# Kernel optimization log

Measured on AMD Instinct MI355X. Metric: run time of the kernel, lower is better.

The kernel has to match this reference:

```python
import jax, jax.numpy as jnp
import numpy as np

RADIUS = 0.1
NSAMPLE = 32


def ball_query_cnt(radius, nsample, xyz, new_xyz):
    """xyz: (B,N,3), new_xyz: (B,npoint,3) -> cnt (B,npoint) int32, idx (B,npoint,nsample) int32.
    Matches pointnet2 CUDA semantics: first `nsample` in-radius points in index order;
    unfilled slots replicate the first found index (0 if none found)."""
    N = xyz.shape[1]
    # (B, npoint, N) squared distances
    d2 = jnp.sum((new_xyz[:, :, None, :] - xyz[:, None, :, :]) ** 2, axis=-1)
    mask = d2 < radius * radius
    pos = jnp.arange(N, dtype=jnp.int32)
    # key encodes position so that top_k returns the LOWEST valid positions first
    key = jnp.where(mask, N - pos, -N)
    topk_vals, _ = jax.lax.top_k(key, nsample)          # (B, npoint, nsample)
    valid = topk_vals > 0
    idx = (N - topk_vals).astype(jnp.int32)
    first = jnp.where(valid[..., :1], idx[..., :1], 0)   # fill value per query
    idx = jnp.where(valid, idx, first)
    cnt = jnp.minimum(mask.sum(axis=-1), nsample).astype(jnp.int32)
    return cnt, idx


def group(features, idx):
    """features: (B,C,N), idx: (B,npoint,nsample) -> (B,C,npoint,nsample)."""
    return jax.vmap(lambda f, i: f[:, i])(features, idx)


def setup_inputs() -> dict:
    key = jax.random.key(0)
    k1, k2, k3 = jax.random.split(key, 3)
    B, N, npoint, C = 4, 16384, 2048, 64
    xyz = jax.random.uniform(k1, (B, N, 3), dtype=jnp.float32)
    new_xyz = jax.random.uniform(k2, (B, npoint, 3), dtype=jnp.float32)
    features = jax.random.normal(k3, (B, C, N), dtype=jnp.float32)
    return {"xyz": xyz, "new_xyz": new_xyz, "features": features}


def reference(xyz, new_xyz, features):
    idx_cnt, idx = ball_query_cnt(RADIUS, NSAMPLE, xyz, new_xyz)
    xyz_t = jnp.transpose(xyz, (0, 2, 1))                      # (B,3,N)
    grouped_xyz = group(xyz_t, idx)                            # (B,3,npoint,nsample)
    grouped_xyz = grouped_xyz - jnp.transpose(new_xyz, (0, 2, 1))[..., None]
    grouped_features = group(features, idx)                    # (B,C,npoint,nsample)
    new_features = jnp.concatenate([grouped_xyz, grouped_features], axis=1)
    return idx_cnt, new_features
```

## Files before the change

kernel.cpp:

```cpp
#include <hip/hip_runtime.h>

#define B        4
#define N        16384
#define NPOINT   2048
#define C        64
#define NSAMPLE  32
#define CH       (C + 3)
#define RADIUS2  0.01f
#define NCELL    1000
#define CSTRIDE  1032
#define CCSTRIDE 1024
#define CAP      256

__device__ __forceinline__ int clamp10(int v) {
    return v < 0 ? 0 : (v > 9 ? 9 : v);
}

__global__ __launch_bounds__(256) void zero_kernel(int* __restrict__ p, int n) {
    const int i = blockIdx.x * 256 + threadIdx.x;
    if (i < n) p[i] = 0;
}

__global__ __launch_bounds__(256) void count_kernel(const float* __restrict__ xyz,
                                                    int* __restrict__ cnt) {
    const int g = blockIdx.x * 256 + threadIdx.x;
    const int b = g >> 14;
    const float x = xyz[g * 3 + 0], y = xyz[g * 3 + 1], z = xyz[g * 3 + 2];
    const int cx = clamp10((int)(x * 10.f));
    const int cy = clamp10((int)(y * 10.f));
    const int cz = clamp10((int)(z * 10.f));
    atomicAdd(&cnt[(b << 10) + (cx * 10 + cy) * 10 + cz], 1);
}

__global__ __launch_bounds__(1024) void prefix_kernel(int* __restrict__ cnt,
                                                      int* __restrict__ cs) {
    __shared__ int s[1024];
    const int t = threadIdx.x, b = blockIdx.x;
    const int v = (t < NCELL) ? cnt[(b << 10) + t] : 0;
    s[t] = v;
    __syncthreads();
    for (int off = 1; off < 1024; off <<= 1) {
        const int u = (t >= off) ? s[t - off] : 0;
        __syncthreads();
        s[t] += u;
        __syncthreads();
    }
    const int excl = (t == 0) ? 0 : s[t - 1];
    if (t <= NCELL) cs[b * CSTRIDE + t] = excl;
    if (t < NCELL)  cnt[(b << 10) + t] = excl;
}

__global__ __launch_bounds__(256) void scatter_kernel(const float* __restrict__ xyz,
                                                      int* __restrict__ cursor,
                                                      float4* __restrict__ sp) {
    const int g = blockIdx.x * 256 + threadIdx.x;
    const int b = g >> 14;
    const int n = g & (N - 1);
    const float x = xyz[g * 3 + 0], y = xyz[g * 3 + 1], z = xyz[g * 3 + 2];
    const int cx = clamp10((int)(x * 10.f));
    const int cy = clamp10((int)(y * 10.f));
    const int cz = clamp10((int)(z * 10.f));
    const int cell = (cx * 10 + cy) * 10 + cz;
    const int pos = atomicAdd(&cursor[(b << 10) + cell], 1);
    sp[(b << 14) + pos] = make_float4(x, y, z, __int_as_float(n));
}

__global__ __launch_bounds__(256) void feat_transpose_kernel(
    const float* __restrict__ f,
    float* __restrict__ ft)
{
    __shared__ float tile[64][65];
    const int b  = blockIdx.y;
    const int n0 = blockIdx.x * 64;
    const int t  = threadIdx.x;
    const int r16 = t >> 4;
    const int x4  = t & 15;
    #pragma unroll
    for (int it = 0; it < 4; ++it) {
        const int cc = it * 16 + r16;
        const float4 v = *(const float4*)(f + ((size_t)b * C + cc) * N + n0 + x4 * 4);
        tile[cc][x4 * 4 + 0] = v.x;
        tile[cc][x4 * 4 + 1] = v.y;
        tile[cc][x4 * 4 + 2] = v.z;
        tile[cc][x4 * 4 + 3] = v.w;
    }
    __syncthreads();
    #pragma unroll
    for (int it = 0; it < 4; ++it) {
        const int nn = it * 16 + r16;
        float4 v;
        v.x = tile[x4 * 4 + 0][nn];
        v.y = tile[x4 * 4 + 1][nn];
        v.z = tile[x4 * 4 + 2][nn];
        v.w = tile[x4 * 4 + 3][nn];
        *(float4*)(ft + ((size_t)b * N + n0 + nn) * C + x4 * 4) = v;
    }
}

__global__ __launch_bounds__(64) void qg_grid_kernel(
    const float*  __restrict__ xyz,
    const float*  __restrict__ new_xyz,
    const float*  __restrict__ ft,
    const int*    __restrict__ cs,
    const float4* __restrict__ sp,
    float* __restrict__ out_cnt,
    float* __restrict__ out_feat)
{
    const int q = blockIdx.x;
    const int b = q >> 11;
    const int j = q & (NPOINT - 1);
    const int l = threadIdx.x;

    __shared__ int   cand[CAP];
    __shared__ int   s_idx[NSAMPLE];
    __shared__ float s_tile[CH * 33];

    const float qx = new_xyz[q * 3 + 0];
    const float qy = new_xyz[q * 3 + 1];
    const float qz = new_xyz[q * 3 + 2];

    const int cx = clamp10((int)(qx * 10.f));
    const int cy = clamp10((int)(qy * 10.f));
    const int cz = clamp10((int)(qz * 10.f));
    const int z0 = cz > 0 ? cz - 1 : 0;
    const int z1 = cz < 9 ? cz + 1 : 9;

    int sv = 0, ev = 0;
    if (l < 9) {
        const int xx = cx - 1 + l / 3;
        const int yy = cy - 1 + l % 3;
        if (xx >= 0 && xx <= 9 && yy >= 0 && yy <= 9) {
            const int cb = (xx * 10 + yy) * 10;
            sv = cs[b * CSTRIDE + cb + z0];
            ev = cs[b * CSTRIDE + cb + z1 + 1];
        }
    }

    const unsigned long long ltmask = (1ull << l) - 1ull;
    int total = 0, ncand = 0;
    for (int r = 0; r < 9; ++r) {
        const int rs = __shfl(sv, r);
        const int re = __shfl(ev, r);
        for (int p0 = rs; p0 < re; p0 += 64) {
            const int p = p0 + l;
            const bool act = p < re;
            float4 pt = make_float4(1e9f, 1e9f, 1e9f, 0.f);
            if (act) pt = sp[(b << 14) + p];
            const float dx = pt.x - qx, dy = pt.y - qy, dz = pt.z - qz;
            const float d2 = dx * dx + dy * dy + dz * dz;
            const bool in = act && (d2 < RADIUS2);
            const unsigned long long m = __ballot(in);
            if (in) {
                const int slot = ncand + __popcll(m & ltmask);
                if (slot < CAP) cand[slot] = __float_as_int(pt.w);
            }
            const int c = __popcll(m);
            total += c;
            ncand = ncand + c > CAP ? CAP : ncand + c;
        }
    }

    int cntv;
    if (total > CAP) {
        const float* xb = xyz + (size_t)b * N * 3;
        int cnt2 = 0;
        for (int base = 0; base < N; base += 64) {
            const int p = base + l;
            const float dx = xb[p * 3 + 0] - qx;
            const float dy = xb[p * 3 + 1] - qy;
            const float dz = xb[p * 3 + 2] - qz;
            const float d2 = dx * dx + dy * dy + dz * dz;
            const bool in = d2 < RADIUS2;
            const unsigned long long m = __ballot(in);
            if (in) {
                const int slot = cnt2 + __popcll(m & ltmask);
                if (slot < NSAMPLE) s_idx[slot] = p;
            }
            cnt2 += __popcll(m);
            if (cnt2 >= NSAMPLE) break;
        }
        cntv = cnt2 < NSAMPLE ? cnt2 : NSAMPLE;
        __syncthreads();
    } else {
        __syncthreads();
        const int K = ncand;
        for (int c = l; c < K; c += 64) {
            const int v = cand[c];
            int rnk = 0;
            for (int i = 0; i < K; ++i) rnk += (cand[i] < v) ? 1 : 0;
            if (rnk < NSAMPLE) s_idx[rnk] = v;
        }
        cntv = total < NSAMPLE ? total : NSAMPLE;
        __syncthreads();
    }

    if (l == 0) out_cnt[q] = (float)cntv;
    if (l < NSAMPLE && l >= cntv) s_idx[l] = (cntv > 0) ? s_idx[0] : 0;
    __syncthreads();

    #pragma unroll
    for (int p = 0; p < 8; ++p) {
        const int k  = p * 4 + (l >> 4);
        const int c4 = l & 15;
        const int i  = s_idx[k];
        const float4 v = ((const float4*)(ft + ((size_t)b * N + i) * C))[c4];
        const int ch = 3 + c4 * 4;
        s_tile[(ch + 0) * 33 + k] = v.x;
        s_tile[(ch + 1) * 33 + k] = v.y;
        s_tile[(ch + 2) * 33 + k] = v.z;
        s_tile[(ch + 3) * 33 + k] = v.w;
    }
    if (l < NSAMPLE) {
        const int i = s_idx[l];
        const float* xp = xyz + ((size_t)b * N + i) * 3;
        s_tile[0 * 33 + l] = xp[0] - qx;
        s_tile[1 * 33 + l] = xp[1] - qy;
        s_tile[2 * 33 + l] = xp[2] - qz;
    }
    __syncthreads();

    float4* of4 = (float4*)out_feat;
    for (int e4 = l; e4 < CH * 8; e4 += 64) {
        const int ch = e4 >> 3;
        const int k4 = e4 & 7;
        float4 v;
        v.x = s_tile[ch * 33 + k4 * 4 + 0];
        v.y = s_tile[ch * 33 + k4 * 4 + 1];
        v.z = s_tile[ch * 33 + k4 * 4 + 2];
        v.w = s_tile[ch * 33 + k4 * 4 + 3];
        of4[((size_t)(b * CH + ch) * NPOINT + j) * 8 + k4] = v;
    }
}

template <bool TRANSPOSED>
__global__ __launch_bounds__(64) void qg_wave_kernel(
    const float* __restrict__ xyz,
    const float* __restrict__ new_xyz,
    const float* __restrict__ feat,
    float* __restrict__ out_cnt,
    float* __restrict__ out_feat)
{
    const int q = blockIdx.x;
    const int b = q >> 11;
    const int j = q & (NPOINT - 1);
    const int l = threadIdx.x;

    __shared__ int   s_idx[NSAMPLE];
    __shared__ float s_tile[CH * 33];

    const float qx = new_xyz[q * 3 + 0];
    const float qy = new_xyz[q * 3 + 1];
    const float qz = new_xyz[q * 3 + 2];
    const float* xb = xyz + (size_t)b * N * 3;

    int cnt = 0;
    for (int base = 0; base < N; base += 64) {
        const int p = base + l;
        const float dx = xb[p * 3 + 0] - qx;
        const float dy = xb[p * 3 + 1] - qy;
        const float dz = xb[p * 3 + 2] - qz;
        const float d2 = dx * dx + dy * dy + dz * dz;
        const bool in = d2 < RADIUS2;
        const unsigned long long m = __ballot(in);
        if (in) {
            const int slot = cnt + __popcll(m & ((1ull << l) - 1ull));
            if (slot < NSAMPLE) s_idx[slot] = p;
        }
        cnt += __popcll(m);
        if (cnt >= NSAMPLE) break;
    }
    if (cnt > NSAMPLE) cnt = NSAMPLE;

    if (l == 0) out_cnt[q] = (float)cnt;
    __syncthreads();
    if (l < NSAMPLE && l >= cnt) s_idx[l] = (cnt > 0) ? s_idx[0] : 0;
    __syncthreads();

    #pragma unroll
    for (int p = 0; p < 8; ++p) {
        const int k  = p * 4 + (l >> 4);
        const int c4 = l & 15;
        const int i  = s_idx[k];
        if (TRANSPOSED) {
            const float4 v = ((const float4*)(feat + ((size_t)b * N + i) * C))[c4];
            const int ch = 3 + c4 * 4;
            s_tile[(ch + 0) * 33 + k] = v.x;
            s_tile[(ch + 1) * 33 + k] = v.y;
            s_tile[(ch + 2) * 33 + k] = v.z;
            s_tile[(ch + 3) * 33 + k] = v.w;
        } else {
            #pragma unroll
            for (int cc = 0; cc < 4; ++cc) {
                const int c = c4 * 4 + cc;
                s_tile[(3 + c) * 33 + k] = feat[((size_t)b * C + c) * N + i];
            }
        }
    }
    if (l < NSAMPLE) {
        const int i = s_idx[l];
        const float* xp = xyz + ((size_t)b * N + i) * 3;
        s_tile[0 * 33 + l] = xp[0] - qx;
        s_tile[1 * 33 + l] = xp[1] - qy;
        s_tile[2 * 33 + l] = xp[2] - qz;
    }
    __syncthreads();

    float4* of4 = (float4*)out_feat;
    for (int e4 = l; e4 < CH * 8; e4 += 64) {
        const int ch = e4 >> 3;
        const int k4 = e4 & 7;
        float4 v;
        v.x = s_tile[ch * 33 + k4 * 4 + 0];
        v.y = s_tile[ch * 33 + k4 * 4 + 1];
        v.z = s_tile[ch * 33 + k4 * 4 + 2];
        v.w = s_tile[ch * 33 + k4 * 4 + 3];
        of4[((size_t)(b * CH + ch) * NPOINT + j) * 8 + k4] = v;
    }
}

extern "C" void kernel_launch(void* const* d_in, const int* in_sizes, int n_in,
                              void* d_out, int out_size, void* d_ws, size_t ws_size,
                              hipStream_t stream) {
    const float* xyz      = (const float*)d_in[0];
    const float* new_xyz  = (const float*)d_in[1];
    const float* features = (const float*)d_in[2];

    float* out_cnt  = (float*)d_out;
    float* out_feat = out_cnt + (size_t)B * NPOINT;

    char* ws = (char*)d_ws;
    const size_t ftB = (size_t)B * N * C * sizeof(float);
    const size_t spB = (size_t)B * N * sizeof(float4);
    const size_t csB = (size_t)B * CSTRIDE * sizeof(int);
    const size_t ccB = (size_t)B * CCSTRIDE * sizeof(int);
    const size_t need = ftB + spB + csB + ccB;

    if (ws_size >= need) {
        float*  ft = (float*)ws;
        float4* sp = (float4*)(ws + ftB);
        int*    cs = (int*)(ws + ftB + spB);
        int*    cc = (int*)(ws + ftB + spB + csB);
        zero_kernel<<<(B * CCSTRIDE + 255) / 256, 256, 0, stream>>>(cc, B * CCSTRIDE);
        count_kernel<<<B * N / 256, 256, 0, stream>>>(xyz, cc);
        prefix_kernel<<<B, 1024, 0, stream>>>(cc, cs);
        scatter_kernel<<<B * N / 256, 256, 0, stream>>>(xyz, cc, sp);
        feat_transpose_kernel<<<dim3(N / 64, B), 256, 0, stream>>>(features, ft);
        qg_grid_kernel<<<B * NPOINT, 64, 0, stream>>>(xyz, new_xyz, ft, cs, sp,
                                                      out_cnt, out_feat);
    } else if (ws_size >= ftB) {
        float* ft = (float*)ws;
        feat_transpose_kernel<<<dim3(N / 64, B), 256, 0, stream>>>(features, ft);
        qg_wave_kernel<true><<<B * NPOINT, 64, 0, stream>>>(xyz, new_xyz, ft,
                                                            out_cnt, out_feat);
    } else {
        qg_wave_kernel<false><<<B * NPOINT, 64, 0, stream>>>(xyz, new_xyz, features,
                                                             out_cnt, out_feat);
    }
}
```

Before: 126.3 us.

## Split ball query from grouping, flatten cell scan, pack four queries per block

The fused query+group kernel becomes two kernels: a ball-query kernel that writes indices to a workspace buffer, and a group kernel that gathers features. Both run four wave-sized queries per 256-thread block with per-wave shared memory, replacing __syncthreads with block fences. The 9-cell candidate scan is flattened into one loop over the concatenated ranges to cut partial-wave iterations. Zeroing of the cell counters is folded into the feature transpose kernel, the candidate cap is reduced, and outputs use nontemporal stores. The extra index round trip through global memory and the reliance on wave-level ordering in place of barriers are the costs and risks.

```diff
diff --git a/kernel.cpp b/kernel.cpp
--- a/kernel.cpp
+++ b/kernel.cpp
@@ -10,15 +10,48 @@
 #define NCELL    1000
 #define CSTRIDE  1032
 #define CCSTRIDE 1024
-#define CAP      256
+#define CAP      192
+
+typedef float vfloat4 __attribute__((ext_vector_type(4)));
 
 __device__ __forceinline__ int clamp10(int v) {
     return v < 0 ? 0 : (v > 9 ? 9 : v);
 }
 
-__global__ __launch_bounds__(256) void zero_kernel(int* __restrict__ p, int n) {
-    const int i = blockIdx.x * 256 + threadIdx.x;
-    if (i < n) p[i] = 0;
+__global__ __launch_bounds__(256) void feat_transpose_zero_kernel(
+    const float* __restrict__ f,
+    float* __restrict__ ft,
+    int* __restrict__ cc)
+{
+    if (blockIdx.y == 0 && blockIdx.x < (B * CCSTRIDE) / 256)
+        cc[blockIdx.x * 256 + threadIdx.x] = 0;
+
+    __shared__ float tile[64][65];
+    const int b  = blockIdx.y;
+    const int n0 = blockIdx.x * 64;
+    const int t  = threadIdx.x;
+    const int r16 = t >> 4;
+    const int x4  = t & 15;
+    #pragma unroll
+    for (int it = 0; it < 4; ++it) {
+        const int cc_ = it * 16 + r16;
+        const float4 v = *(const float4*)(f + ((size_t)b * C + cc_) * N + n0 + x4 * 4);
+        tile[cc_][x4 * 4 + 0] = v.x;
+        tile[cc_][x4 * 4 + 1] = v.y;
+        tile[cc_][x4 * 4 + 2] = v.z;
+        tile[cc_][x4 * 4 + 3] = v.w;
+    }
+    __syncthreads();
+    #pragma unroll
+    for (int it = 0; it < 4; ++it) {
+        const int nn = it * 16 + r16;
+        float4 v;
+        v.x = tile[x4 * 4 + 0][nn];
+        v.y = tile[x4 * 4 + 1][nn];
+        v.z = tile[x4 * 4 + 2][nn];
+        v.w = tile[x4 * 4 + 3][nn];
+        *(float4*)(ft + ((size_t)b * N + n0 + nn) * C + x4 * 4) = v;
+    }
 }
 
 __global__ __launch_bounds__(256) void count_kernel(const float* __restrict__ xyz,
@@ -65,55 +98,23 @@
     sp[(b << 14) + pos] = make_float4(x, y, z, __int_as_float(n));
 }
 
-__global__ __launch_bounds__(256) void feat_transpose_kernel(
-    const float* __restrict__ f,
-    float* __restrict__ ft)
-{
-    __shared__ float tile[64][65];
-    const int b  = blockIdx.y;
-    const int n0 = blockIdx.x * 64;
-    const int t  = threadIdx.x;
-    const int r16 = t >> 4;
-    const int x4  = t & 15;
-    #pragma unroll
-    for (int it = 0; it < 4; ++it) {
-        const int cc = it * 16 + r16;
-        const float4 v = *(const float4*)(f + ((size_t)b * C + cc) * N + n0 + x4 * 4);
-        tile[cc][x4 * 4 + 0] = v.x;
-        tile[cc][x4 * 4 + 1] = v.y;
-        tile[cc][x4 * 4 + 2] = v.z;
-        tile[cc][x4 * 4 + 3] = v.w;
-    }
-    __syncthreads();
-    #pragma unroll
-    for (int it = 0; it < 4; ++it) {
-        const int nn = it * 16 + r16;
-        float4 v;
-        v.x = tile[x4 * 4 + 0][nn];
-        v.y = tile[x4 * 4 + 1][nn];
-        v.z = tile[x4 * 4 + 2][nn];
-        v.w = tile[x4 * 4 + 3][nn];
-        *(float4*)(ft + ((size_t)b * N + n0 + nn) * C + x4 * 4) = v;
-    }
-}
-
-__global__ __launch_bounds__(64) void qg_grid_kernel(
+__global__ __launch_bounds__(256, 8) void ballquery_kernel(
     const float*  __restrict__ xyz,
     const float*  __restrict__ new_xyz,
-    const float*  __restrict__ ft,
     const int*    __restrict__ cs,
     const float4* __restrict__ sp,
     float* __restrict__ out_cnt,
-    float* __restrict__ out_feat)
+    int*   __restrict__ idx_out)
 {
-    const int q = blockIdx.x;
+    const int w = threadIdx.x >> 6;
+    const int l = threadIdx.x & 63;
+    const int q = blockIdx.x * 4 + w;
     const int b = q >> 11;
-    const int j = q & (NPOINT - 1);
-    const int l = threadIdx.x;
-
-    __shared__ int   cand[CAP];
-    __shared__ int   s_idx[NSAMPLE];
-    __shared__ float s_tile[CH * 33];
+
+    __shared__ int cand_s[4][CAP];
+    __shared__ int sidx_s[4][NSAMPLE];
+    int* cand  = cand_s[w];
+    int* s_idx = sidx_s[w];
 
     const float qx = new_xyz[q * 3 + 0];
     const float qy = new_xyz[q * 3 + 1];
@@ -135,29 +136,43 @@
             ev = cs[b * CSTRIDE + cb + z1 + 1];
         }
     }
+    const int len = ev - sv;
+
+    int S[9], L[9];
+    #pragma unroll
+    for (int r = 0; r < 9; ++r) {
+        S[r] = __builtin_amdgcn_readlane(sv, r);
+        L[r] = __builtin_amdgcn_readlane(len, r);
+    }
+    int T = 0;
+    #pragma unroll
+    for (int r = 0; r < 9; ++r) T += L[r];
 
     const unsigned long long ltmask = (1ull << l) - 1ull;
     int total = 0, ncand = 0;
-    for (int r = 0; r < 9; ++r) {
-        const int rs = __shfl(sv, r);
-        const int re = __shfl(ev, r);
-        for (int p0 = rs; p0 < re; p0 += 64) {
-            const int p = p0 + l;
-            const bool act = p < re;
-            float4 pt = make_float4(1e9f, 1e9f, 1e9f, 0.f);
-            if (act) pt = sp[(b << 14) + p];
-            const float dx = pt.x - qx, dy = pt.y - qy, dz = pt.z - qz;
-            const float d2 = dx * dx + dy * dy + dz * dz;
-            const bool in = act && (d2 < RADIUS2);
-            const unsigned long long m = __ballot(in);
-            if (in) {
-                const int slot = ncand + __popcll(m & ltmask);
-                if (slot < CAP) cand[slot] = __float_as_int(pt.w);
-            }
-            const int c = __popcll(m);
-            total += c;
-            ncand = ncand + c > CAP ? CAP : ncand + c;
-        }
+    for (int base = 0; base < T; base += 64) {
+        const int wid = base + l;
+        int p = 0, acc = 0;
+        bool act = false;
+        #pragma unroll
+        for (int r = 0; r < 9; ++r) {
+            const int off = wid - acc;
+            if (off >= 0 && off < L[r]) { p = S[r] + off; act = true; }
+            acc += L[r];
+        }
+        float4 pt = make_float4(1e9f, 1e9f, 1e9f, 0.f);
+        if (act) pt = sp[(b << 14) + p];
+        const float dx = pt.x - qx, dy = pt.y - qy, dz = pt.z - qz;
+        const float d2 = dx * dx + dy * dy + dz * dz;
+        const bool in = act && (d2 < RADIUS2);
+        const unsigned long long m = __ballot(in);
+        if (in) {
+            const int slot = ncand + __popcll(m & ltmask);
+            if (slot < CAP) cand[slot] = __float_as_int(pt.w);
+        }
+        const int c = __popcll(m);
+        total += c;
+        ncand = ncand + c > CAP ? CAP : ncand + c;
     }
 
     int cntv;
@@ -180,9 +195,9 @@
             if (cnt2 >= NSAMPLE) break;
         }
         cntv = cnt2 < NSAMPLE ? cnt2 : NSAMPLE;
-        __syncthreads();
+        __threadfence_block();
     } else {
-        __syncthreads();
+        __threadfence_block();
         const int K = ncand;
         for (int c = l; c < K; c += 64) {
             const int v = cand[c];
@@ -191,12 +206,36 @@
             if (rnk < NSAMPLE) s_idx[rnk] = v;
         }
         cntv = total < NSAMPLE ? total : NSAMPLE;
-        __syncthreads();
-    }
+        __threadfence_block();
+    }
+
+    if (l < NSAMPLE && l >= cntv) s_idx[l] = (cntv > 0) ? s_idx[0] : 0;
+    __threadfence_block();
 
     if (l == 0) out_cnt[q] = (float)cntv;
-    if (l < NSAMPLE && l >= cntv) s_idx[l] = (cntv > 0) ? s_idx[0] : 0;
-    __syncthreads();
+    if (l < NSAMPLE) idx_out[q * NSAMPLE + l] = s_idx[l];
+}
+
+__global__ __launch_bounds__(256, 4) void group_kernel(
+    const float* __restrict__ xyz,
+    const float* __restrict__ new_xyz,
+    const float* __restrict__ ft,
+    const int*   __restrict__ idx_in,
+    float* __restrict__ out_feat)
+{
+    const int w = threadIdx.x >> 6;
+    const int l = threadIdx.x & 63;
+    const int q = blockIdx.x * 4 + w;
+    const int b = q >> 11;
+    const int j = q & (NPOINT - 1);
+
+    __shared__ float tile_s[4][CH * 33];
+    __shared__ int   sidx_s[4][NSAMPLE];
+    float* s_tile = tile_s[w];
+    int*   s_idx  = sidx_s[w];
+
+    if (l < NSAMPLE) s_idx[l] = idx_in[q * NSAMPLE + l];
+    __threadfence_block();
 
     #pragma unroll
     for (int p = 0; p < 8; ++p) {
@@ -211,24 +250,27 @@
         s_tile[(ch + 3) * 33 + k] = v.w;
     }
     if (l < NSAMPLE) {
+        const float qx = new_xyz[q * 3 + 0];
+        const float qy = new_xyz[q * 3 + 1];
+        const float qz = new_xyz[q * 3 + 2];
         const int i = s_idx[l];
         const float* xp = xyz + ((size_t)b * N + i) * 3;
         s_tile[0 * 33 + l] = xp[0] - qx;
         s_tile[1 * 33 + l] = xp[1] - qy;
         s_tile[2 * 33 + l] = xp[2] - qz;
     }
-    __syncthreads();
-
-    float4* of4 = (float4*)out_feat;
+    __threadfence_block();
+
+    vfloat4* of4 = (vfloat4*)out_feat;
     for (int e4 = l; e4 < CH * 8; e4 += 64) {
         const int ch = e4 >> 3;
         const int k4 = e4 & 7;
-        float4 v;
+        vfloat4 v;
         v.x = s_tile[ch * 33 + k4 * 4 + 0];
         v.y = s_tile[ch * 33 + k4 * 4 + 1];
         v.z = s_tile[ch * 33 + k4 * 4 + 2];
         v.w = s_tile[ch * 33 + k4 * 4 + 3];
-        of4[((size_t)(b * CH + ch) * NPOINT + j) * 8 + k4] = v;
+        __builtin_nontemporal_store(v, &of4[((size_t)(b * CH + ch) * NPOINT + j) * 8 + k4]);
     }
 }
 
@@ -329,27 +371,31 @@
     float* out_feat = out_cnt + (size_t)B * NPOINT;
 
     char* ws = (char*)d_ws;
-    const size_t ftB = (size_t)B * N * C * sizeof(float);
-    const size_t spB = (size_t)B * N * sizeof(float4);
-    const size_t csB = (size_t)B * CSTRIDE * sizeof(int);
-    const size_t ccB = (size_t)B * CCSTRIDE * sizeof(int);
-    const size_t need = ftB + spB + csB + ccB;
+    const size_t ftB  = (size_t)B * N * C * sizeof(float);
+    const size_t spB  = (size_t)B * N * sizeof(float4);
+    const size_t csB  = (size_t)B * CSTRIDE * sizeof(int);
+    const size_t ccB  = (size_t)B * CCSTRIDE * sizeof(int);
+    const size_t idxB = (size_t)B * NPOINT * NSAMPLE * sizeof(int);
+    const size_t need = ftB + spB + csB + ccB + idxB;
 
     if (ws_size >= need) {
-        float*  ft = (float*)ws;
-        float4* sp = (float4*)(ws + ftB);
-        int*    cs = (int*)(ws + ftB + spB);
-        int*    cc = (int*)(ws + ftB + spB + csB);
-        zero_kernel<<<(B * CCSTRIDE + 255) / 256, 256, 0, stream>>>(cc, B * CCSTRIDE);
+        float*  ft  = (float*)ws;
+        float4* sp  = (float4*)(ws + ftB);
+        int*    cs  = (int*)(ws + ftB + spB);
+        int*    cc  = (int*)(ws + ftB + spB + csB);
+        int*    idx = (int*)(ws + ftB + spB + csB + ccB);
+        feat_transpose_zero_kernel<<<dim3(N / 64, B), 256, 0, stream>>>(features, ft, cc);
         count_kernel<<<B * N / 256, 256, 0, stream>>>(xyz, cc);
         prefix_kernel<<<B, 1024, 0, stream>>>(cc, cs);
         scatter_kernel<<<B * N / 256, 256, 0, stream>>>(xyz, cc, sp);
-        feat_transpose_kernel<<<dim3(N / 64, B), 256, 0, stream>>>(features, ft);
-        qg_grid_kernel<<<B * NPOINT, 64, 0, stream>>>(xyz, new_xyz, ft, cs, sp,
-                                                      out_cnt, out_feat);
+        ballquery_kernel<<<B * NPOINT / 4, 256, 0, stream>>>(xyz, new_xyz, cs, sp,
+                                                             out_cnt, idx);
+        group_kernel<<<B * NPOINT / 4, 256, 0, stream>>>(xyz, new_xyz, ft, idx,
+                                                         out_feat);
     } else if (ws_size >= ftB) {
         float* ft = (float*)ws;
-        feat_transpose_kernel<<<dim3(N / 64, B), 256, 0, stream>>>(features, ft);
+        feat_transpose_zero_kernel<<<dim3(N / 64, B), 256, 0, stream>>>(
+            features, ft, (int*)(ws + ftB - (size_t)B * CCSTRIDE * sizeof(int)));
         qg_wave_kernel<true><<<B * NPOINT, 64, 0, stream>>>(xyz, new_xyz, ft,
                                                             out_cnt, out_feat);
     } else {
```

Result: slower. 133.5 us (+5.7%).

## Fuse grid-build and transpose into one prep kernel, pack four queries per block

Applied to the files above, without the earlier changes.

The zero, count, prefix, scatter and feature-transpose kernels are merged into one prep kernel. Four blocks build each batch's cell histogram, prefix sum and scatter in shared memory, and the remaining blocks do the transpose. The query kernel now runs four one-wave queries per 256-thread block, with wave-local fences in place of block barriers. It walks the nine cell ranges as one flattened loop, uses a smaller candidate cap, and writes output with nontemporal stores. The goal is to cut launch overhead and global atomics and to improve occupancy. In exchange, the per-batch serial histogram block runs with little parallelism, and correctness now relies on single-wave LDS ordering.

```diff
diff --git a/kernel.cpp b/kernel.cpp
--- a/kernel.cpp
+++ b/kernel.cpp
@@ -9,95 +9,105 @@
 #define RADIUS2  0.01f
 #define NCELL    1000
 #define CSTRIDE  1032
-#define CCSTRIDE 1024
-#define CAP      256
+#define CAP      192
+
+typedef float vfloat4 __attribute__((ext_vector_type(4)));
 
 __device__ __forceinline__ int clamp10(int v) {
     return v < 0 ? 0 : (v > 9 ? 9 : v);
 }
 
-__global__ __launch_bounds__(256) void zero_kernel(int* __restrict__ p, int n) {
-    const int i = blockIdx.x * 256 + threadIdx.x;
-    if (i < n) p[i] = 0;
-}
-
-__global__ __launch_bounds__(256) void count_kernel(const float* __restrict__ xyz,
-                                                    int* __restrict__ cnt) {
-    const int g = blockIdx.x * 256 + threadIdx.x;
-    const int b = g >> 14;
-    const float x = xyz[g * 3 + 0], y = xyz[g * 3 + 1], z = xyz[g * 3 + 2];
-    const int cx = clamp10((int)(x * 10.f));
-    const int cy = clamp10((int)(y * 10.f));
-    const int cz = clamp10((int)(z * 10.f));
-    atomicAdd(&cnt[(b << 10) + (cx * 10 + cy) * 10 + cz], 1);
-}
-
-__global__ __launch_bounds__(1024) void prefix_kernel(int* __restrict__ cnt,
-                                                      int* __restrict__ cs) {
-    __shared__ int s[1024];
-    const int t = threadIdx.x, b = blockIdx.x;
-    const int v = (t < NCELL) ? cnt[(b << 10) + t] : 0;
-    s[t] = v;
-    __syncthreads();
-    for (int off = 1; off < 1024; off <<= 1) {
-        const int u = (t >= off) ? s[t - off] : 0;
-        __syncthreads();
-        s[t] += u;
-        __syncthreads();
-    }
-    const int excl = (t == 0) ? 0 : s[t - 1];
-    if (t <= NCELL) cs[b * CSTRIDE + t] = excl;
-    if (t < NCELL)  cnt[(b << 10) + t] = excl;
-}
-
-__global__ __launch_bounds__(256) void scatter_kernel(const float* __restrict__ xyz,
-                                                      int* __restrict__ cursor,
-                                                      float4* __restrict__ sp) {
-    const int g = blockIdx.x * 256 + threadIdx.x;
-    const int b = g >> 14;
-    const int n = g & (N - 1);
-    const float x = xyz[g * 3 + 0], y = xyz[g * 3 + 1], z = xyz[g * 3 + 2];
-    const int cx = clamp10((int)(x * 10.f));
-    const int cy = clamp10((int)(y * 10.f));
-    const int cz = clamp10((int)(z * 10.f));
-    const int cell = (cx * 10 + cy) * 10 + cz;
-    const int pos = atomicAdd(&cursor[(b << 10) + cell], 1);
-    sp[(b << 14) + pos] = make_float4(x, y, z, __int_as_float(n));
-}
-
-__global__ __launch_bounds__(256) void feat_transpose_kernel(
+__global__ __launch_bounds__(256) void prep_kernel(
+    const float* __restrict__ xyz,
     const float* __restrict__ f,
-    float* __restrict__ ft)
+    float* __restrict__ ft,
+    int* __restrict__ cs,
+    float4* __restrict__ sp)
 {
-    __shared__ float tile[64][65];
-    const int b  = blockIdx.y;
-    const int n0 = blockIdx.x * 64;
-    const int t  = threadIdx.x;
-    const int r16 = t >> 4;
-    const int x4  = t & 15;
-    #pragma unroll
-    for (int it = 0; it < 4; ++it) {
-        const int cc = it * 16 + r16;
-        const float4 v = *(const float4*)(f + ((size_t)b * C + cc) * N + n0 + x4 * 4);
-        tile[cc][x4 * 4 + 0] = v.x;
-        tile[cc][x4 * 4 + 1] = v.y;
-        tile[cc][x4 * 4 + 2] = v.z;
-        tile[cc][x4 * 4 + 3] = v.w;
-    }
-    __syncthreads();
-    #pragma unroll
-    for (int it = 0; it < 4; ++it) {
-        const int nn = it * 16 + r16;
-        float4 v;
-        v.x = tile[x4 * 4 + 0][nn];
-        v.y = tile[x4 * 4 + 1][nn];
-        v.z = tile[x4 * 4 + 2][nn];
-        v.w = tile[x4 * 4 + 3][nn];
-        *(float4*)(ft + ((size_t)b * N + n0 + nn) * C + x4 * 4) = v;
-    }
-}
-
-__global__ __launch_bounds__(64) void qg_grid_kernel(
+    const int t = threadIdx.x;
+
+    if (blockIdx.x < B) {
+        const int b = blockIdx.x;
+        const float* xb = xyz + (size_t)b * N * 3;
+
+        __shared__ int hist[1024];
+        __shared__ int wsum[256];
+
+        hist[t] = 0; hist[256 + t] = 0; hist[512 + t] = 0; hist[768 + t] = 0;
+        __syncthreads();
+
+        for (int g = t; g < N; g += 256) {
+            const int cx = clamp10((int)(xb[g * 3 + 0] * 10.f));
+            const int cy = clamp10((int)(xb[g * 3 + 1] * 10.f));
+            const int cz = clamp10((int)(xb[g * 3 + 2] * 10.f));
+            atomicAdd(&hist[(cx * 10 + cy) * 10 + cz], 1);
+        }
+        __syncthreads();
+
+        const int h0 = hist[t * 4 + 0], h1 = hist[t * 4 + 1];
+        const int h2 = hist[t * 4 + 2], h3 = hist[t * 4 + 3];
+        wsum[t] = h0 + h1 + h2 + h3;
+        __syncthreads();
+        for (int off = 1; off < 256; off <<= 1) {
+            const int u = (t >= off) ? wsum[t - off] : 0;
+            __syncthreads();
+            wsum[t] += u;
+            __syncthreads();
+        }
+        const int base = (t == 0) ? 0 : wsum[t - 1];
+        const int c0 = base, c1 = c0 + h0, c2 = c1 + h1, c3 = c2 + h2;
+        __syncthreads();
+        hist[t * 4 + 0] = c0;
+        hist[t * 4 + 1] = c1;
+        hist[t * 4 + 2] = c2;
+        hist[t * 4 + 3] = c3;
+        int* csb = cs + b * CSTRIDE;
+        csb[t * 4 + 0] = c0;
+        csb[t * 4 + 1] = c1;
+        csb[t * 4 + 2] = c2;
+        csb[t * 4 + 3] = c3;
+        __syncthreads();
+
+        for (int g = t; g < N; g += 256) {
+            const float x = xb[g * 3 + 0], y = xb[g * 3 + 1], z = xb[g * 3 + 2];
+            const int cx = clamp10((int)(x * 10.f));
+            const int cy = clamp10((int)(y * 10.f));
+            const int cz = clamp10((int)(z * 10.f));
+            const int pos = atomicAdd(&hist[(cx * 10 + cy) * 10 + cz], 1);
+            sp[(b << 14) + pos] = make_float4(x, y, z, __int_as_float(g));
+        }
+    } else {
+        const int tt = blockIdx.x - B;
+        const int b  = tt >> 8;
+        const int n0 = (tt & 255) * 64;
+
+        __shared__ float tile[64][65];
+        const int r16 = t >> 4;
+        const int x4  = t & 15;
+        #pragma unroll
+        for (int it = 0; it < 4; ++it) {
+            const int cc = it * 16 + r16;
+            const float4 v = *(const float4*)(f + ((size_t)b * C + cc) * N + n0 + x4 * 4);
+            tile[cc][x4 * 4 + 0] = v.x;
+            tile[cc][x4 * 4 + 1] = v.y;
+            tile[cc][x4 * 4 + 2] = v.z;
+            tile[cc][x4 * 4 + 3] = v.w;
+        }
+        __syncthreads();
+        #pragma unroll
+        for (int it = 0; it < 4; ++it) {
+            const int nn = it * 16 + r16;
+            float4 v;
+            v.x = tile[x4 * 4 + 0][nn];
+            v.y = tile[x4 * 4 + 1][nn];
+            v.z = tile[x4 * 4 + 2][nn];
+            v.w = tile[x4 * 4 + 3][nn];
+            *(float4*)(ft + ((size_t)b * N + n0 + nn) * C + x4 * 4) = v;
+        }
+    }
+}
+
+__global__ __launch_bounds__(256, 4) void qg_kernel(
     const float*  __restrict__ xyz,
     const float*  __restrict__ new_xyz,
     const float*  __restrict__ ft,
@@ -106,14 +116,18 @@
     float* __restrict__ out_cnt,
     float* __restrict__ out_feat)
 {
-    const int q = blockIdx.x;
+    const int w = threadIdx.x >> 6;
+    const int l = threadIdx.x & 63;
+    const int q = blockIdx.x * 4 + w;
     const int b = q >> 11;
     const int j = q & (NPOINT - 1);
-    const int l = threadIdx.x;
-
-    __shared__ int   cand[CAP];
-    __shared__ int   s_idx[NSAMPLE];
-    __shared__ float s_tile[CH * 33];
+
+    __shared__ int   cand_s[4][CAP];
+    __shared__ int   sidx_s[4][NSAMPLE];
+    __shared__ float tile_s[4][CH * 33];
+    int*   cand   = cand_s[w];
+    int*   s_idx  = sidx_s[w];
+    float* s_tile = tile_s[w];
 
     const float qx = new_xyz[q * 3 + 0];
     const float qy = new_xyz[q * 3 + 1];
@@ -135,29 +149,43 @@
             ev = cs[b * CSTRIDE + cb + z1 + 1];
         }
     }
+    const int len = ev - sv;
+
+    int S[9], L[9];
+    #pragma unroll
+    for (int r = 0; r < 9; ++r) {
+        S[r] = __builtin_amdgcn_readlane(sv, r);
+        L[r] = __builtin_amdgcn_readlane(len, r);
+    }
+    int T = 0;
+    #pragma unroll
+    for (int r = 0; r < 9; ++r) T += L[r];
 
     const unsigned long long ltmask = (1ull << l) - 1ull;
     int total = 0, ncand = 0;
-    for (int r = 0; r < 9; ++r) {
-        const int rs = __shfl(sv, r);
-        const int re = __shfl(ev, r);
-        for (int p0 = rs; p0 < re; p0 += 64) {
-            const int p = p0 + l;
-            const bool act = p < re;
-            float4 pt = make_float4(1e9f, 1e9f, 1e9f, 0.f);
-            if (act) pt = sp[(b << 14) + p];
-            const float dx = pt.x - qx, dy = pt.y - qy, dz = pt.z - qz;
-            const float d2 = dx * dx + dy * dy + dz * dz;
-            const bool in = act && (d2 < RADIUS2);
-            const unsigned long long m = __ballot(in);
-            if (in) {
-                const int slot = ncand + __popcll(m & ltmask);
-                if (slot < CAP) cand[slot] = __float_as_int(pt.w);
-            }
-            const int c = __popcll(m);
-            total += c;
-            ncand = ncand + c > CAP ? CAP : ncand + c;
-        }
+    for (int base = 0; base < T; base += 64) {
+        const int wid = base + l;
+        int p = 0, acc = 0;
+        bool act = false;
+        #pragma unroll
+        for (int r = 0; r < 9; ++r) {
+            const int off = wid - acc;
+            if (off >= 0 && off < L[r]) { p = S[r] + off; act = true; }
+            acc += L[r];
+        }
+        float4 pt = make_float4(1e9f, 1e9f, 1e9f, 0.f);
+        if (act) pt = sp[(b << 14) + p];
+        const float dx = pt.x - qx, dy = pt.y - qy, dz = pt.z - qz;
+        const float d2 = dx * dx + dy * dy + dz * dz;
+        const bool in = act && (d2 < RADIUS2);
+        const unsigned long long m = __ballot(in);
+        if (in) {
+            const int slot = ncand + __popcll(m & ltmask);
+            if (slot < CAP) cand[slot] = __float_as_int(pt.w);
+        }
+        const int c = __popcll(m);
+        total += c;
+        ncand = ncand + c > CAP ? CAP : ncand + c;
     }
 
     int cntv;
@@ -180,9 +208,9 @@
             if (cnt2 >= NSAMPLE) break;
         }
         cntv = cnt2 < NSAMPLE ? cnt2 : NSAMPLE;
-        __syncthreads();
+        __threadfence_block();
     } else {
-        __syncthreads();
+        __threadfence_block();
         const int K = ncand;
         for (int c = l; c < K; c += 64) {
             const int v = cand[c];
@@ -191,12 +219,13 @@
             if (rnk < NSAMPLE) s_idx[rnk] = v;
         }
         cntv = total < NSAMPLE ? total : NSAMPLE;
-        __syncthreads();
-    }
+        __threadfence_block();
+    }
+
+    if (l < NSAMPLE && l >= cntv) s_idx[l] = (cntv > 0) ? s_idx[0] : 0;
+    __threadfence_block();
 
     if (l == 0) out_cnt[q] = (float)cntv;
-    if (l < NSAMPLE && l >= cntv) s_idx[l] = (cntv > 0) ? s_idx[0] : 0;
-    __syncthreads();
 
     #pragma unroll
     for (int p = 0; p < 8; ++p) {
@@ -217,22 +246,21 @@
         s_tile[1 * 33 + l] = xp[1] - qy;
         s_tile[2 * 33 + l] = xp[2] - qz;
     }
-    __syncthreads();
-
-    float4* of4 = (float4*)out_feat;
+    __threadfence_block();
+
+    vfloat4* of4 = (vfloat4*)out_feat;
     for (int e4 = l; e4 < CH * 8; e4 += 64) {
         const int ch = e4 >> 3;
         const int k4 = e4 & 7;
-        float4 v;
+        vfloat4 v;
         v.x = s_tile[ch * 33 + k4 * 4 + 0];
         v.y = s_tile[ch * 33 + k4 * 4 + 1];
         v.z = s_tile[ch * 33 + k4 * 4 + 2];
         v.w = s_tile[ch * 33 + k4 * 4 + 3];
-        of4[((size_t)(b * CH + ch) * NPOINT + j) * 8 + k4] = v;
-    }
-}
-
-template <bool TRANSPOSED>
+        __builtin_nontemporal_store(v, &of4[((size_t)(b * CH + ch) * NPOINT + j) * 8 + k4]);
+    }
+}
+
 __global__ __launch_bounds__(64) void qg_wave_kernel(
     const float* __restrict__ xyz,
     const float* __restrict__ new_xyz,
@@ -281,19 +309,10 @@
         const int k  = p * 4 + (l >> 4);
         const int c4 = l & 15;
         const int i  = s_idx[k];
-        if (TRANSPOSED) {
-            const float4 v = ((const float4*)(feat + ((size_t)b * N + i) * C))[c4];
-            const int ch = 3 + c4 * 4;
-            s_tile[(ch + 0) * 33 + k] = v.x;
-            s_tile[(ch + 1) * 33 + k] = v.y;
-            s_tile[(ch + 2) * 33 + k] = v.z;
-            s_tile[(ch + 3) * 33 + k] = v.w;
-        } else {
-            #pragma unroll
-            for (int cc = 0; cc < 4; ++cc) {
-                const int c = c4 * 4 + cc;
-                s_tile[(3 + c) * 33 + k] = feat[((size_t)b * C + c) * N + i];
-            }
+        #pragma unroll
+        for (int cc = 0; cc < 4; ++cc) {
+            const int c = c4 * 4 + cc;
+            s_tile[(3 + c) * 33 + k] = feat[((size_t)b * C + c) * N + i];
         }
     }
     if (l < NSAMPLE) {
@@ -332,28 +351,17 @@
     const size_t ftB = (size_t)B * N * C * sizeof(float);
     const size_t spB = (size_t)B * N * sizeof(float4);
     const size_t csB = (size_t)B * CSTRIDE * sizeof(int);
-    const size_t ccB = (size_t)B * CCSTRIDE * sizeof(int);
-    const size_t need = ftB + spB + csB + ccB;
+    const size_t need = ftB + spB + csB;
 
     if (ws_size >= need) {
         float*  ft = (float*)ws;
         float4* sp = (float4*)(ws + ftB);
         int*    cs = (int*)(ws + ftB + spB);
-        int*    cc = (int*)(ws + ftB + spB + csB);
-        zero_kernel<<<(B * CCSTRIDE + 255) / 256, 256, 0, stream>>>(cc, B * CCSTRIDE);
-        count_kernel<<<B * N / 256, 256, 0, stream>>>(xyz, cc);
-        prefix_kernel<<<B, 1024, 0, stream>>>(cc, cs);
-        scatter_kernel<<<B * N / 256, 256, 0, stream>>>(xyz, cc, sp);
-        feat_transpose_kernel<<<dim3(N / 64, B), 256, 0, stream>>>(features, ft);
-        qg_grid_kernel<<<B * NPOINT, 64, 0, stream>>>(xyz, new_xyz, ft, cs, sp,
+        prep_kernel<<<B + B * (N / 64), 256, 0, stream>>>(xyz, features, ft, cs, sp);
+        qg_kernel<<<B * NPOINT / 4, 256, 0, stream>>>(xyz, new_xyz, ft, cs, sp,
                                                       out_cnt, out_feat);
-    } else if (ws_size >= ftB) {
-        float* ft = (float*)ws;
-        feat_transpose_kernel<<<dim3(N / 64, B), 256, 0, stream>>>(features, ft);
-        qg_wave_kernel<true><<<B * NPOINT, 64, 0, stream>>>(xyz, new_xyz, ft,
-                                                            out_cnt, out_feat);
     } else {
-        qg_wave_kernel<false><<<B * NPOINT, 64, 0, stream>>>(xyz, new_xyz, features,
-                                                             out_cnt, out_feat);
-    }
-}
+        qg_wave_kernel<<<B * NPOINT, 64, 0, stream>>>(xyz, new_xyz, features,
+                                                      out_cnt, out_feat);
+    }
+}
```

After: 161.6 us. +28.0%, slower.
